# Kernel optimization log

Hardware: AMD Instinct MI355X
Metric: run time of the kernel (lower is better)

## Reference

```python
import jax, jax.numpy as jnp
import numpy as np

KH, KW, STRIDE, PAD, DIL = 3, 3, 1, 1, 1


def setup_inputs() -> dict:
    key = jax.random.key(0)
    ks = jax.random.split(key, 4)
    B, C, H, W, O = 4, 256, 64, 64, 256
    K = KH * KW
    x = jax.random.normal(ks[0], (B, C, H, W), jnp.float32)
    # offset/mask conv params (original inits to zero; use small random so offsets are non-trivial)
    w_om = jax.random.normal(ks[1], (3 * K, C, KH, KW), jnp.float32) * 0.01
    b_om = jnp.zeros((3 * K,), jnp.float32)
    # main weight: kaiming_uniform_(a=1) -> gain = sqrt(2/(1+1^2)) = 1, bound = sqrt(3)/sqrt(fan_in)
    fan_in = C * K
    bound = float(np.sqrt(3.0) / np.sqrt(fan_in))
    weight = jax.random.uniform(ks[2], (O, C, KH, KW), jnp.float32, -bound, bound)
    bias = jnp.zeros((O,), jnp.float32)
    return {"x": x, "w_om": w_om, "b_om": b_om, "weight": weight, "bias": bias}


def _deform_conv2d(x, offset, mask, weight, bias):
    # torchvision.ops.deform_conv2d semantics, deformable_groups=1, stride=1, pad=1, dil=1
    B, C, H, W = x.shape
    K = KH * KW
    # torchvision offset layout: per-tap interleaved (y, x) pairs along channel dim
    off_y = offset[:, 0::2]  # [B, K, H, W]
    off_x = offset[:, 1::2]  # [B, K, H, W]
    ky = (jnp.repeat(jnp.arange(KH), KW) * DIL).astype(x.dtype)  # [K]
    kx = (jnp.tile(jnp.arange(KW), KH) * DIL).astype(x.dtype)    # [K]
    base_y = (jnp.arange(H) * STRIDE - PAD).astype(x.dtype)
    base_x = (jnp.arange(W) * STRIDE - PAD).astype(x.dtype)
    py = base_y[None, None, :, None] + ky[None, :, None, None] + off_y  # [B,K,H,W]
    px = base_x[None, None, None, :] + kx[None, :, None, None] + off_x  # [B,K,H,W]
    y0 = jnp.floor(py)
    x0 = jnp.floor(px)
    ly = py - y0
    lx = px - x0
    y0i = y0.astype(jnp.int32)
    x0i = x0.astype(jnp.int32)
    x_flat = x.reshape(B, C, H * W)

    def gather(yy, xx):
        # zero-padded gather of one bilinear corner -> [B, C, K, H, W]
        valid = ((yy >= 0) & (yy < H) & (xx >= 0) & (xx < W)).astype(x.dtype)
        idx = (jnp.clip(yy, 0, H - 1) * W + jnp.clip(xx, 0, W - 1)).reshape(B, -1)
        g = jax.vmap(lambda xf, i: jnp.take(xf, i, axis=1))(x_flat, idx)
        return g.reshape(B, C, K, H, W) * valid.reshape(B, 1, K, H, W)

    w00 = ((1 - ly) * (1 - lx))[:, None]
    w01 = ((1 - ly) * lx)[:, None]
    w10 = (ly * (1 - lx))[:, None]
    w11 = (ly * lx)[:, None]
    val = (gather(y0i, x0i) * w00 + gather(y0i, x0i + 1) * w01
           + gather(y0i + 1, x0i) * w10 + gather(y0i + 1, x0i + 1) * w11)
    cols = val * mask[:, None]  # modulated columns [B,C,K,H,W]
    out = jnp.einsum('bckhw,ock->bohw', cols, weight.reshape(weight.shape[0], C, K))
    return out + bias[None, :, None, None]


def reference(x, w_om, b_om, weight, bias):
    om = jax.lax.conv_general_dilated(
        x, w_om, (STRIDE, STRIDE), ((PAD, PAD), (PAD, PAD)),
        rhs_dilation=(DIL, DIL), dimension_numbers=('NCHW', 'OIHW', 'NCHW'),
    ) + b_om[None, :, None, None]
    K = KH * KW
    o1, o2, m = om[:, :K], om[:, K:2 * K], om[:, 2 * K:]
    offset = jnp.concatenate([o1, o2], axis=1)  # [B, 2K, H, W]
    mask = jax.nn.sigmoid(m)                    # [B, K, H, W]
    return _deform_conv2d(x, offset, mask, weight, bias)
```

## Files before the change

kernel.cpp:

```cpp
#include <hip/hip_runtime.h>
#include <stdint.h>

#define B_ 4
#define C_ 256
#define H_ 64
#define W_ 64
#define O_ 256
#define K_ 9
#define CK 2304
#define HW 4096
#define NTOT 16384

typedef __bf16 bf16x8 __attribute__((ext_vector_type(8)));
typedef __bf16 bf16x4 __attribute__((ext_vector_type(4)));
typedef float f32x4 __attribute__((ext_vector_type(4)));
typedef float f32x2 __attribute__((ext_vector_type(2)));
typedef f32x2 __attribute__((aligned(4))) f32x2u;

__device__ __forceinline__ uint16_t f2bf(float f) {
  uint32_t u = __builtin_bit_cast(uint32_t, f);
  return (uint16_t)((u + 0x7FFFu + ((u >> 16) & 1u)) >> 16);
}

__device__ __forceinline__ uint32_t pk_bf16(float a, float b) {
  uint16_t lo = __builtin_bit_cast(uint16_t, (__bf16)a);
  uint16_t hi = __builtin_bit_cast(uint16_t, (__bf16)b);
  return (uint32_t)lo | ((uint32_t)hi << 16);
}

__global__ void kA_prep(const float* __restrict__ weight, const float* __restrict__ w_om,
                        const float* __restrict__ x, uint16_t* __restrict__ wb,
                        uint16_t* __restrict__ womb, uint16_t* __restrict__ xT) {
  int bx = blockIdx.x;
  int t = threadIdx.x;
  if (bx < 2304) {
    int idx = bx * 256 + t;
    int o = idx / CK;
    int rem = idx - o * CK;
    int k = rem >> 8, c = rem & 255;
    wb[idx] = f2bf(weight[(o * C_ + c) * K_ + k]);
  } else if (bx < 2592) {
    int idx = (bx - 2304) * 256 + t;
    int j = idx / CK;
    int ck = idx - j * CK;
    int k = ck >> 8, c = ck & 255;
    womb[idx] = (j < 27) ? f2bf(w_om[(j * 256 + c) * 9 + k]) : (uint16_t)0;
  } else {
    int bxl = bx - 2592;
    int ct = bxl & 3;
    int hwt = (bxl >> 2) & 63;
    int b = bxl >> 8;
    int l = t & 63;
    int cq = t >> 6;

    __shared__ __align__(16) uint16_t tile[64 * 72];

    const float* xb = x + ((b * 256 + ct * 64) * HW) + hwt * 64;
#pragma unroll
    for (int i = 0; i < 16; ++i) {
      int c = cq * 16 + i;
      tile[l * 72 + c] = f2bf(xb[c * HW + l]);
    }
    __syncthreads();

    int hw = t >> 2;
    int c8 = (t & 3) * 8;
    uint16_t* dst = xT + ((size_t)b << 20) + (size_t)(hwt * 64 + hw) * 256 + ct * 64;
    *(uint4*)&dst[c8] = *(const uint4*)&tile[hw * 72 + c8];
    *(uint4*)&dst[c8 + 32] = *(const uint4*)&tile[hw * 72 + c8 + 32];
  }
}

__device__ __forceinline__ void write_om(float v, int j, int n, const float* __restrict__ b_om,
                                         float* __restrict__ pypxmk) {
  if (j >= 27) return;
  float s = v + b_om[j];
  int b = n >> 12, hw = n & 4095;
  int h = hw >> 6, w = hw & 63;
  if (j < 18) {
    int k = j >> 1;
    int off = (b * 9 + k) * HW + hw;
    if ((j & 1) == 0)
      pypxmk[off] = (float)(h - 1 + k / 3) + s;
    else
      pypxmk[147456 + off] = (float)(w - 1 + k % 3) + s;
  } else {
    int k = j - 18;
    pypxmk[294912 + (b * 9 + k) * HW + hw] = 1.f / (1.f + __expf(-s));
  }
}

__global__ void k1_mfma(const uint16_t* __restrict__ womb, const uint16_t* __restrict__ xT,
                        const float* __restrict__ b_om, float* __restrict__ pypxmk) {
  int nt = blockIdx.x;
  int t = threadIdx.x;
  int lane = t & 63;
  int wid = t >> 6;
  int lr = lane & 15, q = lane >> 4;
  int n = nt * 64 + wid * 16 + lr;
  int b = n >> 12;
  int hw = n & 4095;
  int y = hw >> 6, xx = hw & 63;
  const uint16_t* xb = xT + ((size_t)b << 20);
  const uint16_t* zrow = womb + 31 * CK;

  f32x4 acc0 = {0.f, 0.f, 0.f, 0.f};
  f32x4 acc1 = {0.f, 0.f, 0.f, 0.f};

#pragma unroll
  for (int k = 0; k < 9; ++k) {
    int dy = k / 3, dx = k - dy * 3;
    int ny = y + dy - 1, nx = xx + dx - 1;
    bool valid = ((unsigned)ny < 64u) && ((unsigned)nx < 64u);
    int row = (min(max(ny, 0), 63) << 6) + min(max(nx, 0), 63);
    const uint16_t* bp = valid ? (xb + row * 256 + q * 8) : (zrow + q * 8);
    const uint16_t* ap = womb + lr * CK + k * 256 + q * 8;
#pragma unroll
    for (int kt = 0; kt < 8; ++kt) {
      int c0 = kt * 32;
      bf16x8 bF = *(const bf16x8*)&bp[c0];
      bf16x8 aF0 = *(const bf16x8*)&ap[c0];
      bf16x8 aF1 = *(const bf16x8*)&ap[16 * CK + c0];
      acc0 = __builtin_amdgcn_mfma_f32_16x16x32_bf16(aF0, bF, acc0, 0, 0, 0);
      acc1 = __builtin_amdgcn_mfma_f32_16x16x32_bf16(aF1, bF, acc1, 0, 0, 0);
    }
  }

#pragma unroll
  for (int r = 0; r < 4; ++r) {
    write_om(acc0[r], q * 4 + r, n, b_om, pypxmk);
    write_om(acc1[r], 16 + q * 4 + r, n, b_om, pypxmk);
  }
}


struct GatherState {
  float wa0[4], wb0[4], wa1[4], wb1[4];
  bf16x4 r00[4], r01[4], r10[4], r11[4];
};

__device__ __forceinline__ void gather_issue(GatherState& S, const uint16_t* __restrict__ xb,
                                             const float* __restrict__ pyA,
                                             const float* __restrict__ pxA,
                                             const float* __restrict__ mkA,
                                             int b, int kg, int n0, int rbase, int lane) {
#pragma unroll
  for (int j = 0; j < 4; ++j) {
    int nrow = rbase + j;
    int poff = (b * 9 + kg) * HW + ((n0 + nrow) & 4095);
    float py = pyA[poff];
    float px = pxA[poff];
    float mk = mkA[poff];
    float fy0 = floorf(py), fx0 = floorf(px);
    float ly = py - fy0, lx = px - fx0;
    int y0 = (int)fy0, x0 = (int)fx0;
    bool vy0 = ((unsigned)y0 < 64u), vy1 = ((unsigned)(y0 + 1) < 64u);
    bool vx0 = ((unsigned)x0 < 64u), vx1 = ((unsigned)(x0 + 1) < 64u);
    float w00 = (vy0 && vx0) ? (1.f - ly) * (1.f - lx) * mk : 0.f;
    float w01 = (vy0 && vx1) ? (1.f - ly) * lx * mk : 0.f;
    float w10 = (vy1 && vx0) ? ly * (1.f - lx) * mk : 0.f;
    float w11 = (vy1 && vx1) ? ly * lx * mk : 0.f;
    bool sel0 = (x0 >= 63);
    bool sel1 = (x0 >= 0);
    S.wa0[j] = (sel0 ? 0.f : w00) + (sel1 ? 0.f : w01);
    S.wb0[j] = (sel0 ? w00 : 0.f) + (sel1 ? w01 : 0.f);
    S.wa1[j] = (sel0 ? 0.f : w10) + (sel1 ? 0.f : w11);
    S.wb1[j] = (sel0 ? w10 : 0.f) + (sel1 ? w11 : 0.f);
    int bx0 = min(max(x0, 0), 62);
    int a0 = min(max(y0, 0), 63) * 64 + bx0;
    int a1 = min(max(y0 + 1, 0), 63) * 64 + bx0;
    S.r00[j] = *(const bf16x4*)&xb[a0 * 256 + lane * 4];
    S.r01[j] = *(const bf16x4*)&xb[a0 * 256 + 256 + lane * 4];
    S.r10[j] = *(const bf16x4*)&xb[a1 * 256 + lane * 4];
    S.r11[j] = *(const bf16x4*)&xb[a1 * 256 + 256 + lane * 4];
  }
}

__device__ __forceinline__ void gather_finish(const GatherState& S, uint16_t* bslab,
                                              int rbase, int lane) {
#pragma unroll
  for (int j = 0; j < 4; ++j) {
    int nrow = rbase + j;
    float v[4];
#pragma unroll
    for (int i = 0; i < 4; ++i)
      v[i] = S.wa0[j] * (float)S.r00[j][i] + S.wb0[j] * (float)S.r01[j][i] +
             S.wa1[j] * (float)S.r10[j][i] + S.wb1[j] * (float)S.r11[j][i];
    uint2 pk;
    pk.x = pk_bf16(v[0], v[1]);
    pk.y = pk_bf16(v[2], v[3]);
    int chunk = lane >> 1;
    int chs = (chunk & 24) | ((chunk & 7) ^ (nrow & 7));
    *(uint2*)&bslab[nrow * 256 + chs * 8 + (lane & 1) * 4] = pk;
  }
}

__device__ __forceinline__ void stageA(const uint16_t* __restrict__ wb, uint16_t* asbuf,
                                       int kbase, int t) {
#pragma unroll
  for (int i = 0; i < 4; ++i) {
    int rr = i * 64 + (t >> 3);
    const uint16_t* src = wb + rr * CK + kbase + (((t & 7) ^ (rr & 7)) << 3);
    __builtin_amdgcn_global_load_lds(
        (const __attribute__((address_space(1))) uint32_t*)src,
        (__attribute__((address_space(3))) uint32_t*)&asbuf[i * 4096 + t * 8], 16, 0, 0);
  }
}

__device__ __forceinline__ void mma_step(const uint16_t* AsP, const uint16_t* BsP,
                                         f32x4 acc[4][2], int wm, int wn, int lr, int q,
                                         int kt2) {
#pragma unroll
  for (int kc = 0; kc < 2; ++kc) {
    bf16x8 aF[4], bF[2];
#pragma unroll
    for (int i = 0; i < 4; ++i) {
      int row = wm * 64 + i * 16 + lr;
      aF[i] = *(const bf16x8*)&AsP[row * 64 + (((kc * 4 + q) ^ (row & 7)) << 3)];
    }
#pragma unroll
    for (int j = 0; j < 2; ++j) {
      int row = wn * 32 + j * 16 + lr;
      int kidx = kt2 * 8 + kc * 4 + q;
      int chs = (kidx & 24) | ((kidx & 7) ^ (row & 7));
      bF[j] = *(const bf16x8*)&BsP[row * 256 + chs * 8];
    }
#pragma unroll
    for (int i = 0; i < 4; ++i)
#pragma unroll
      for (int j = 0; j < 2; ++j)
        acc[i][j] = __builtin_amdgcn_mfma_f32_16x16x32_bf16(aF[i], bF[j], acc[i][j], 0, 0, 0);
  }
}

__global__ __launch_bounds__(512, 2) void k23_fused(const uint16_t* __restrict__ wb,
                                                    const uint16_t* __restrict__ xT,
                                                    const float* __restrict__ pypxmk,
                                                    const float* __restrict__ bias,
                                                    float* __restrict__ out) {
  __shared__ __align__(16) uint16_t As[2][16384];
  __shared__ __align__(16) uint16_t Bs[16384];

  int t = threadIdx.x;
  int lane = t & 63;
  int wid = __builtin_amdgcn_readfirstlane(t >> 6);
  int lr = lane & 15, q = lane >> 4;
  int wm = wid >> 1, wn = wid & 1;
  int bx = blockIdx.x;
  int swz = (bx & 7) * 32 + (bx >> 3);
  int n0 = swz * 64;
  int b = n0 >> 12;
  int hw0 = n0 & 4095;
  const uint16_t* xb = xT + ((size_t)b << 20);
  const float* pyA = pypxmk;
  const float* pxA = pypxmk + 147456;
  const float* mkA = pypxmk + 294912;

  f32x4 acc[4][2];
  const f32x4 zero = {0.f, 0.f, 0.f, 0.f};
#pragma unroll
  for (int i = 0; i < 4; ++i)
#pragma unroll
    for (int j = 0; j < 2; ++j) acc[i][j] = zero;

  GatherState S;
  int wrow = wid * 8;

  gather_issue(S, xb, pyA, pxA, mkA, b, 0, n0, wrow, lane);
  gather_finish(S, Bs, wrow, lane);
  gather_issue(S, xb, pyA, pxA, mkA, b, 0, n0, wrow + 4, lane);
  gather_finish(S, Bs, wrow + 4, lane);
  stageA(wb, As[0], 0, t);
  __syncthreads();

  for (int k = 0; k < 9; ++k) {
    for (int kt2 = 0; kt2 < 4; ++kt2) {
      if (!(k == 8 && kt2 == 3)) {
        int kb2 = (kt2 == 3) ? (k + 1) * 256 : k * 256 + (kt2 + 1) * 64;
        stageA(wb, As[(kt2 + 1) & 1], kb2, t);
      }
      mma_step(As[kt2 & 1], Bs, acc, wm, wn, lr, q, kt2);
      __syncthreads();
    }
    if (k < 8) {
      gather_issue(S, xb, pyA, pxA, mkA, b, k + 1, n0, wrow, lane);
      gather_finish(S, Bs, wrow, lane);
      gather_issue(S, xb, pyA, pxA, mkA, b, k + 1, n0, wrow + 4, lane);
      gather_finish(S, Bs, wrow + 4, lane);
      __syncthreads();
    }
  }

#pragma unroll
  for (int i = 0; i < 4; ++i) {
#pragma unroll
    for (int r = 0; r < 4; ++r) {
      int o = wm * 64 + i * 16 + q * 4 + r;
      float bv = bias[o];
      float* orow = out + (b * O_ + o) * HW + hw0;
#pragma unroll
      for (int j = 0; j < 2; ++j) orow[wn * 32 + j * 16 + lr] = acc[i][j][r] + bv;
    }
  }
}

__global__ void k0_wconv(const float* __restrict__ weight, uint16_t* __restrict__ wb) {
  int idx = blockIdx.x * 256 + threadIdx.x;
  if (idx >= O_ * CK) return;
  int o = idx / CK;
  int rem = idx - o * CK;
  int k = rem >> 8;
  int c = rem & 255;
  wb[idx] = f2bf(weight[(o * C_ + c) * K_ + k]);
}

__global__ void k1_offconv(const float* __restrict__ x, const float* __restrict__ w_om,
                           const float* __restrict__ b_om, float* __restrict__ pypxmk) {
  int bx = blockIdx.x;
  int jq = bx % 7;
  int h = (bx / 7) % H_;
  int b = bx / (7 * H_);
  int t = threadIdx.x;
  int w = t & 63;
  int cs = __builtin_amdgcn_readfirstlane(t >> 6);

  float acc[4] = {0.f, 0.f, 0.f, 0.f};
  const float* xb = x + (b * C_) * HW;

  for (int ci = 0; ci < 64; ++ci) {
    int c = cs * 64 + ci;
    const float* xr = xb + c * HW;
    float xv[3][3];
#pragma unroll
    for (int r = 0; r < 3; ++r) {
      int y = h - 1 + r;
      bool yv = ((unsigned)y < 64u);
#pragma unroll
      for (int dx = 0; dx < 3; ++dx) {
        int xx = w - 1 + dx;
        bool v = yv && ((unsigned)xx < 64u);
        xv[r][dx] = v ? xr[y * 64 + xx] : 0.f;
      }
    }
    const float* wp = w_om + ((jq * 4) * C_ + c) * 9;
#pragma unroll
    for (int jj = 0; jj < 4; ++jj) {
      int j = jq * 4 + jj;
      int jeff = (j < 27) ? jj : 0;
      const float* wj = wp + jeff * (C_ * 9);
      float a = 0.f;
#pragma unroll
      for (int r = 0; r < 3; ++r)
#pragma unroll
        for (int dx = 0; dx < 3; ++dx)
          a = fmaf(xv[r][dx], wj[r * 3 + dx], a);
      acc[jj] += a;
    }
  }

  __shared__ float red[4][4][64];
#pragma unroll
  for (int jj = 0; jj < 4; ++jj) red[cs][jj][w] = acc[jj];
  __syncthreads();

  int jj = t >> 6;
  int j = jq * 4 + jj;
  if (j < 27) {
    float s = red[0][jj][w] + red[1][jj][w] + red[2][jj][w] + red[3][jj][w] + b_om[j];
    float* pyA = pypxmk;
    float* pxA = pypxmk + 147456;
    float* mkA = pypxmk + 294912;
    if (j < 18) {
      int k = j >> 1;
      int off = (b * 9 + k) * HW + h * 64 + w;
      if ((j & 1) == 0)
        pyA[off] = (float)(h - 1 + k / 3) + s;
      else
        pxA[off] = (float)(w - 1 + k % 3) + s;
    } else {
      int k = j - 18;
      mkA[(b * 9 + k) * HW + h * 64 + w] = 1.f / (1.f + __expf(-s));
    }
  }
}

__global__ void k2_fb(const float* __restrict__ x, const float* __restrict__ pypxmk,
                      uint16_t* __restrict__ cols) {
  int bx = blockIdx.x;
  int cg = bx & 15;
  int h = (bx >> 4) & 63;
  int b = bx >> 10;
  int t = threadIdx.x;
  int w = t & 63;
  int g = t >> 6;

  const float* pyA = pypxmk;
  const float* pxA = pypxmk + 147456;
  const float* mkA = pypxmk + 294912;

  __shared__ uint16_t tile[64 * 146];
  const float* xb = x + b * C_ * HW;
  int cbase = cg * 16 + g * 4;

#pragma unroll
  for (int k = 0; k < 9; ++k) {
    int poff = (b * 9 + k) * HW + h * 64 + w;
    float py = pyA[poff];
    float px = pxA[poff];
    float mk = mkA[poff];
    float fy0 = floorf(py), fx0 = floorf(px);
    float ly = py - fy0, lx = px - fx0;
    int y0 = (int)fy0, x0 = (int)fx0;
    bool vy0 = ((unsigned)y0 < 64u), vy1 = ((unsigned)(y0 + 1) < 64u);
    bool vx0 = ((unsigned)x0 < 64u), vx1 = ((unsigned)(x0 + 1) < 64u);
    float w00 = (vy0 && vx0) ? (1.f - ly) * (1.f - lx) * mk : 0.f;
    float w01 = (vy0 && vx1) ? (1.f - ly) * lx * mk : 0.f;
    float w10 = (vy1 && vx0) ? ly * (1.f - lx) * mk : 0.f;
    float w11 = (vy1 && vx1) ? ly * lx * mk : 0.f;
    bool sel0 = (x0 >= 63);
    bool sel1 = (x0 >= 0);
    float wa0 = (sel0 ? 0.f : w00) + (sel1 ? 0.f : w01);
    float wb0 = (sel0 ? w00 : 0.f) + (sel1 ? w01 : 0.f);
    float wa1 = (sel0 ? 0.f : w10) + (sel1 ? 0.f : w11);
    float wb1 = (sel0 ? w10 : 0.f) + (sel1 ? w11 : 0.f);
    int bx0 = min(max(x0, 0), 62);
    int a0 = min(max(y0, 0), 63) * 64 + bx0;
    int a1 = min(max(y0 + 1, 0), 63) * 64 + bx0;

#pragma unroll
    for (int cp = 0; cp < 2; ++cp) {
      const float* xcA = xb + (cbase + cp * 2) * HW;
      const float* xcB = xcA + HW;
      f32x2 A0 = *(const f32x2u*)&xcA[a0];
      f32x2 A1 = *(const f32x2u*)&xcA[a1];
      f32x2 B0 = *(const f32x2u*)&xcB[a0];
      f32x2 B1 = *(const f32x2u*)&xcB[a1];
      float rA = wa0 * A0.x + wb0 * A0.y + wa1 * A1.x + wb1 * A1.y;
      float rB = wa0 * B0.x + wb0 * B0.y + wa1 * B1.x + wb1 * B1.y;
      *(uint32_t*)&tile[w * 146 + k * 16 + g * 4 + cp * 2] = pk_bf16(rA, rB);
    }
  }
  __syncthreads();

#pragma unroll
  for (int it = 0; it < 18; ++it) {
    int u = t + it * 256;
    int wu = u / 72;
    int rem = u - wu * 72;
    int k = rem >> 3;
    int cd = rem & 7;
    uint32_t val = *(const uint32_t*)&tile[wu * 146 + rem * 2];
    int n = b * HW + h * 64 + wu;
    int dst = n * CK + k * 256 + cg * 16 + cd * 2;
    *(uint32_t*)&cols[dst] = val;
  }
}

__global__ void k3_flex(const uint16_t* __restrict__ wb, const uint16_t* __restrict__ cols,
                        const float* __restrict__ bias, float* __restrict__ out) {
  int bx = blockIdx.x;
  int mt = bx & 1;
  int nt = bx >> 1;
  int o0 = mt * 128;
  int n0 = nt * 128;
  int t = threadIdx.x;
  int lane = t & 63;
  int wid = t >> 6;
  int wm = wid >> 1, wn = wid & 1;
  int lr = lane & 15, q = lane >> 4;

  __shared__ __align__(16) uint16_t As[128 * 32];
  __shared__ __align__(16) uint16_t Bs[128 * 32];

  f32x4 acc[4][4];
  const f32x4 zero = {0.f, 0.f, 0.f, 0.f};
#pragma unroll
  for (int i = 0; i < 4; ++i)
#pragma unroll
    for (int j = 0; j < 4; ++j) acc[i][j] = zero;

  int r0 = t >> 2;
  int koff = (t & 3) * 8;
  const uint16_t* gA = wb + (o0 + r0) * CK + koff;
  const uint16_t* gB = cols + (n0 + r0) * CK + koff;

  for (int kt = 0; kt < 72; ++kt) {
    int k0 = kt * 32;
    __builtin_amdgcn_global_load_lds(
        (const __attribute__((address_space(1))) uint32_t*)(gA + k0),
        (__attribute__((address_space(3))) uint32_t*)&As[t * 8], 16, 0, 0);
    __builtin_amdgcn_global_load_lds(
        (const __attribute__((address_space(1))) uint32_t*)(gA + 64 * CK + k0),
        (__attribute__((address_space(3))) uint32_t*)&As[2048 + t * 8], 16, 0, 0);
    __builtin_amdgcn_global_load_lds(
        (const __attribute__((address_space(1))) uint32_t*)(gB + k0),
        (__attribute__((address_space(3))) uint32_t*)&Bs[t * 8], 16, 0, 0);
    __builtin_amdgcn_global_load_lds(
        (const __attribute__((address_space(1))) uint32_t*)(gB + 64 * CK + k0),
        (__attribute__((address_space(3))) uint32_t*)&Bs[2048 + t * 8], 16, 0, 0);
    __syncthreads();

    bf16x8 aF[4], bF[4];
#pragma unroll
    for (int i = 0; i < 4; ++i)
      aF[i] = *(const bf16x8*)&As[(wm * 64 + i * 16 + lr) * 32 + q * 8];
#pragma unroll
    for (int j = 0; j < 4; ++j)
      bF[j] = *(const bf16x8*)&Bs[(wn * 64 + j * 16 + lr) * 32 + q * 8];
#pragma unroll
    for (int i = 0; i < 4; ++i)
#pragma unroll
      for (int j = 0; j < 4; ++j)
        acc[i][j] = __builtin_amdgcn_mfma_f32_16x16x32_bf16(aF[i], bF[j], acc[i][j], 0, 0, 0);
    __syncthreads();
  }

  int bb = n0 >> 12;
  int hw0 = n0 & 4095;
#pragma unroll
  for (int i = 0; i < 4; ++i) {
#pragma unroll
    for (int r = 0; r < 4; ++r) {
      int o = o0 + wm * 64 + i * 16 + q * 4 + r;
      float bv = bias[o];
      float* orow = out + (bb * O_ + o) * HW + hw0;
#pragma unroll
      for (int j = 0; j < 4; ++j) orow[wn * 64 + j * 16 + lr] = acc[i][j][r] + bv;
    }
  }
}

extern "C" void kernel_launch(void* const* d_in, const int* in_sizes, int n_in,
                              void* d_out, int out_size, void* d_ws, size_t ws_size,
                              hipStream_t stream) {
  const float* x = (const float*)d_in[0];
  const float* w_om = (const float*)d_in[1];
  const float* b_om = (const float*)d_in[2];
  const float* weight = (const float*)d_in[3];
  const float* bias = (const float*)d_in[4];
  float* out = (float*)d_out;

  char* ws = (char*)d_ws;
  uint16_t* wb = (uint16_t*)ws;
  uint16_t* womb = (uint16_t*)(ws + 1179648);
  uint16_t* xT = (uint16_t*)(ws + 1327104);
  float* pypxmk = (float*)(ws + 9715712);

  if (ws_size >= 11485184ull) {
    hipLaunchKernelGGL(kA_prep, dim3(3616), dim3(256), 0, stream, weight, w_om, x, wb, womb, xT);
    hipLaunchKernelGGL(k1_mfma, dim3(256), dim3(256), 0, stream, womb, xT, b_om, pypxmk);
    hipLaunchKernelGGL(k23_fused, dim3(256), dim3(512), 0, stream, wb, xT, pypxmk, bias, out);
  } else {
    float* pypx_fb = (float*)(ws + 1179648);
    uint16_t* colsf = (uint16_t*)(ws + 2949120);
    hipLaunchKernelGGL(k0_wconv, dim3(2304), dim3(256), 0, stream, weight, wb);
    hipLaunchKernelGGL(k1_offconv, dim3(4 * 64 * 7), dim3(256), 0, stream, x, w_om, b_om, pypx_fb);
    hipLaunchKernelGGL(k2_fb, dim3(4 * 64 * 16), dim3(256), 0, stream, x, pypx_fb, colsf);
    hipLaunchKernelGGL(k3_flex, dim3(256), dim3(256), 0, stream, wb, colsf, bias, out);
  }
}
```

Before: 168.9 us.

## Fuse offset/mask conv into deformable GEMM kernel and compact weight prep

The offset/mask convolution moves out of its own kernel and into the start of the fused gather+GEMM kernel. Each block computes the offsets for its 64 output positions with MFMA, splitting the 9 taps across two wave halves and reducing them through shared memory. The results stay in LDS instead of going through a global pypxmk buffer, which removes one launch and a global round trip. The weight conversion in the prep kernel is also restructured so each thread converts 9 taps per channel, cutting the grid size. The cost is some offset-conv work at the head of each block, which adds latency before the gather pipeline can start.

```diff
diff --git a/kernel.cpp b/kernel.cpp
--- a/kernel.cpp
+++ b/kernel.cpp
@@ -33,20 +33,22 @@
                         uint16_t* __restrict__ womb, uint16_t* __restrict__ xT) {
   int bx = blockIdx.x;
   int t = threadIdx.x;
-  if (bx < 2304) {
-    int idx = bx * 256 + t;
-    int o = idx / CK;
-    int rem = idx - o * CK;
-    int k = rem >> 8, c = rem & 255;
-    wb[idx] = f2bf(weight[(o * C_ + c) * K_ + k]);
-  } else if (bx < 2592) {
-    int idx = (bx - 2304) * 256 + t;
-    int j = idx / CK;
-    int ck = idx - j * CK;
-    int k = ck >> 8, c = ck & 255;
-    womb[idx] = (j < 27) ? f2bf(w_om[(j * 256 + c) * 9 + k]) : (uint16_t)0;
+  if (bx < 256) {
+    int o = bx, c = t;
+    const float* wp = weight + (o * 256 + c) * 9;
+#pragma unroll
+    for (int k = 0; k < 9; ++k) wb[o * CK + k * 256 + c] = f2bf(wp[k]);
+  } else if (bx < 283) {
+    int j = bx - 256, c = t;
+    const float* wp = w_om + (j * 256 + c) * 9;
+#pragma unroll
+    for (int k = 0; k < 9; ++k) womb[j * CK + k * 256 + c] = f2bf(wp[k]);
+  } else if (bx < 288) {
+    int j = 27 + (bx - 283), c = t;
+#pragma unroll
+    for (int k = 0; k < 9; ++k) womb[j * CK + k * 256 + c] = 0;
   } else {
-    int bxl = bx - 2592;
+    int bxl = bx - 288;
     int ct = bxl & 3;
     int hwt = (bxl >> 2) & 63;
     int b = bxl >> 8;
@@ -71,68 +73,6 @@
   }
 }
 
-__device__ __forceinline__ void write_om(float v, int j, int n, const float* __restrict__ b_om,
-                                         float* __restrict__ pypxmk) {
-  if (j >= 27) return;
-  float s = v + b_om[j];
-  int b = n >> 12, hw = n & 4095;
-  int h = hw >> 6, w = hw & 63;
-  if (j < 18) {
-    int k = j >> 1;
-    int off = (b * 9 + k) * HW + hw;
-    if ((j & 1) == 0)
-      pypxmk[off] = (float)(h - 1 + k / 3) + s;
-    else
-      pypxmk[147456 + off] = (float)(w - 1 + k % 3) + s;
-  } else {
-    int k = j - 18;
-    pypxmk[294912 + (b * 9 + k) * HW + hw] = 1.f / (1.f + __expf(-s));
-  }
-}
-
-__global__ void k1_mfma(const uint16_t* __restrict__ womb, const uint16_t* __restrict__ xT,
-                        const float* __restrict__ b_om, float* __restrict__ pypxmk) {
-  int nt = blockIdx.x;
-  int t = threadIdx.x;
-  int lane = t & 63;
-  int wid = t >> 6;
-  int lr = lane & 15, q = lane >> 4;
-  int n = nt * 64 + wid * 16 + lr;
-  int b = n >> 12;
-  int hw = n & 4095;
-  int y = hw >> 6, xx = hw & 63;
-  const uint16_t* xb = xT + ((size_t)b << 20);
-  const uint16_t* zrow = womb + 31 * CK;
-
-  f32x4 acc0 = {0.f, 0.f, 0.f, 0.f};
-  f32x4 acc1 = {0.f, 0.f, 0.f, 0.f};
-
-#pragma unroll
-  for (int k = 0; k < 9; ++k) {
-    int dy = k / 3, dx = k - dy * 3;
-    int ny = y + dy - 1, nx = xx + dx - 1;
-    bool valid = ((unsigned)ny < 64u) && ((unsigned)nx < 64u);
-    int row = (min(max(ny, 0), 63) << 6) + min(max(nx, 0), 63);
-    const uint16_t* bp = valid ? (xb + row * 256 + q * 8) : (zrow + q * 8);
-    const uint16_t* ap = womb + lr * CK + k * 256 + q * 8;
-#pragma unroll
-    for (int kt = 0; kt < 8; ++kt) {
-      int c0 = kt * 32;
-      bf16x8 bF = *(const bf16x8*)&bp[c0];
-      bf16x8 aF0 = *(const bf16x8*)&ap[c0];
-      bf16x8 aF1 = *(const bf16x8*)&ap[16 * CK + c0];
-      acc0 = __builtin_amdgcn_mfma_f32_16x16x32_bf16(aF0, bF, acc0, 0, 0, 0);
-      acc1 = __builtin_amdgcn_mfma_f32_16x16x32_bf16(aF1, bF, acc1, 0, 0, 0);
-    }
-  }
-
-#pragma unroll
-  for (int r = 0; r < 4; ++r) {
-    write_om(acc0[r], q * 4 + r, n, b_om, pypxmk);
-    write_om(acc1[r], 16 + q * 4 + r, n, b_om, pypxmk);
-  }
-}
-
 
 struct GatherState {
   float wa0[4], wb0[4], wa1[4], wb1[4];
@@ -140,17 +80,14 @@
 };
 
 __device__ __forceinline__ void gather_issue(GatherState& S, const uint16_t* __restrict__ xb,
-                                             const float* __restrict__ pyA,
-                                             const float* __restrict__ pxA,
-                                             const float* __restrict__ mkA,
-                                             int b, int kg, int n0, int rbase, int lane) {
+                                             const float* pypx_l,
+                                             int kg, int rbase, int lane) {
 #pragma unroll
   for (int j = 0; j < 4; ++j) {
     int nrow = rbase + j;
-    int poff = (b * 9 + kg) * HW + ((n0 + nrow) & 4095);
-    float py = pyA[poff];
-    float px = pxA[poff];
-    float mk = mkA[poff];
+    float py = pypx_l[(0 * 9 + kg) * 64 + nrow];
+    float px = pypx_l[(1 * 9 + kg) * 64 + nrow];
+    float mk = pypx_l[(2 * 9 + kg) * 64 + nrow];
     float fy0 = floorf(py), fx0 = floorf(px);
     float ly = py - fy0, lx = px - fx0;
     int y0 = (int)fy0, x0 = (int)fx0;
@@ -233,28 +170,90 @@
   }
 }
 
-__global__ __launch_bounds__(512, 2) void k23_fused(const uint16_t* __restrict__ wb,
-                                                    const uint16_t* __restrict__ xT,
-                                                    const float* __restrict__ pypxmk,
-                                                    const float* __restrict__ bias,
-                                                    float* __restrict__ out) {
+__global__ __launch_bounds__(512, 2) void k123(const uint16_t* __restrict__ wb,
+                                               const uint16_t* __restrict__ womb,
+                                               const uint16_t* __restrict__ xT,
+                                               const float* __restrict__ b_om,
+                                               const float* __restrict__ bias,
+                                               float* __restrict__ out) {
   __shared__ __align__(16) uint16_t As[2][16384];
   __shared__ __align__(16) uint16_t Bs[16384];
+  __shared__ float pypx_l[3 * 9 * 64];
 
   int t = threadIdx.x;
   int lane = t & 63;
   int wid = __builtin_amdgcn_readfirstlane(t >> 6);
   int lr = lane & 15, q = lane >> 4;
-  int wm = wid >> 1, wn = wid & 1;
   int bx = blockIdx.x;
   int swz = (bx & 7) * 32 + (bx >> 3);
   int n0 = swz * 64;
   int b = n0 >> 12;
   int hw0 = n0 & 4095;
   const uint16_t* xb = xT + ((size_t)b << 20);
-  const float* pyA = pypxmk;
-  const float* pxA = pypxmk + 147456;
-  const float* mkA = pypxmk + 294912;
+
+  {
+    int ns4 = wid & 3;
+    int kh2 = wid >> 2;
+    int hw = (n0 + ns4 * 16 + lr) & 4095;
+    int y = hw >> 6, xx = hw & 63;
+    const uint16_t* zrow = womb + 31 * CK;
+
+    f32x4 acc0 = {0.f, 0.f, 0.f, 0.f};
+    f32x4 acc1 = {0.f, 0.f, 0.f, 0.f};
+
+    int ks = kh2 ? 4 : 0;
+    int ke = kh2 ? 9 : 4;
+    for (int k = ks; k < ke; ++k) {
+      int dy = k / 3, dx = k - dy * 3;
+      int ny = y + dy - 1, nx = xx + dx - 1;
+      bool valid = ((unsigned)ny < 64u) && ((unsigned)nx < 64u);
+      int row = (min(max(ny, 0), 63) << 6) + min(max(nx, 0), 63);
+      const uint16_t* bp = valid ? (xb + row * 256 + q * 8) : (zrow + q * 8);
+      const uint16_t* ap = womb + lr * CK + k * 256 + q * 8;
+#pragma unroll
+      for (int kt = 0; kt < 8; ++kt) {
+        int c0 = kt * 32;
+        bf16x8 bF = *(const bf16x8*)&bp[c0];
+        bf16x8 aF0 = *(const bf16x8*)&ap[c0];
+        bf16x8 aF1 = *(const bf16x8*)&ap[16 * CK + c0];
+        acc0 = __builtin_amdgcn_mfma_f32_16x16x32_bf16(aF0, bF, acc0, 0, 0, 0);
+        acc1 = __builtin_amdgcn_mfma_f32_16x16x32_bf16(aF1, bF, acc1, 0, 0, 0);
+      }
+    }
+
+    float* red = (float*)As;
+    int base = ((kh2 * 4 + ns4) * 64 + lane) * 8;
+#pragma unroll
+    for (int r = 0; r < 4; ++r) {
+      red[base + r] = acc0[r];
+      red[base + 4 + r] = acc1[r];
+    }
+    __syncthreads();
+
+    if (kh2 == 0) {
+      int b0 = (ns4 * 64 + lane) * 8;
+      int b1 = ((4 + ns4) * 64 + lane) * 8;
+      int nn = ns4 * 16 + lr;
+#pragma unroll
+      for (int i = 0; i < 8; ++i) {
+        float s = red[b0 + i] + red[b1 + i];
+        int j = (i < 4) ? (q * 4 + i) : (16 + q * 4 + (i - 4));
+        if (j < 27) {
+          float v = s + b_om[j];
+          if (j < 18) {
+            int k = j >> 1;
+            if ((j & 1) == 0)
+              pypx_l[(0 * 9 + k) * 64 + nn] = (float)(y - 1 + k / 3) + v;
+            else
+              pypx_l[(1 * 9 + k) * 64 + nn] = (float)(xx - 1 + k % 3) + v;
+          } else {
+            pypx_l[(2 * 9 + (j - 18)) * 64 + nn] = 1.f / (1.f + __expf(-v));
+          }
+        }
+      }
+    }
+    __syncthreads();
+  }
 
   f32x4 acc[4][2];
   const f32x4 zero = {0.f, 0.f, 0.f, 0.f};
@@ -263,12 +262,13 @@
 #pragma unroll
     for (int j = 0; j < 2; ++j) acc[i][j] = zero;
 
+  int wm = wid >> 1, wn = wid & 1;
   GatherState S;
   int wrow = wid * 8;
 
-  gather_issue(S, xb, pyA, pxA, mkA, b, 0, n0, wrow, lane);
+  gather_issue(S, xb, pypx_l, 0, wrow, lane);
   gather_finish(S, Bs, wrow, lane);
-  gather_issue(S, xb, pyA, pxA, mkA, b, 0, n0, wrow + 4, lane);
+  gather_issue(S, xb, pypx_l, 0, wrow + 4, lane);
   gather_finish(S, Bs, wrow + 4, lane);
   stageA(wb, As[0], 0, t);
   __syncthreads();
@@ -283,9 +283,9 @@
       __syncthreads();
     }
     if (k < 8) {
-      gather_issue(S, xb, pyA, pxA, mkA, b, k + 1, n0, wrow, lane);
+      gather_issue(S, xb, pypx_l, k + 1, wrow, lane);
       gather_finish(S, Bs, wrow, lane);
-      gather_issue(S, xb, pyA, pxA, mkA, b, k + 1, n0, wrow + 4, lane);
+      gather_issue(S, xb, pypx_l, k + 1, wrow + 4, lane);
       gather_finish(S, Bs, wrow + 4, lane);
       __syncthreads();
     }
@@ -387,7 +387,7 @@
 __global__ void k2_fb(const float* __restrict__ x, const float* __restrict__ pypxmk,
                       uint16_t* __restrict__ cols) {
   int bx = blockIdx.x;
-  int cg = bx & 15;
+  int cg2 = bx & 15;
   int h = (bx >> 4) & 63;
   int b = bx >> 10;
   int t = threadIdx.x;
@@ -400,7 +400,7 @@
 
   __shared__ uint16_t tile[64 * 146];
   const float* xb = x + b * C_ * HW;
-  int cbase = cg * 16 + g * 4;
+  int cbase = cg2 * 16 + g * 4;
 
 #pragma unroll
   for (int k = 0; k < 9; ++k) {
@@ -451,7 +451,7 @@
     int cd = rem & 7;
     uint32_t val = *(const uint32_t*)&tile[wu * 146 + rem * 2];
     int n = b * HW + h * 64 + wu;
-    int dst = n * CK + k * 256 + cg * 16 + cd * 2;
+    int dst = n * CK + k * 256 + cg2 * 16 + cd * 2;
     *(uint32_t*)&cols[dst] = val;
   }
 }
@@ -544,12 +544,10 @@
   uint16_t* wb = (uint16_t*)ws;
   uint16_t* womb = (uint16_t*)(ws + 1179648);
   uint16_t* xT = (uint16_t*)(ws + 1327104);
-  float* pypxmk = (float*)(ws + 9715712);
 
   if (ws_size >= 11485184ull) {
-    hipLaunchKernelGGL(kA_prep, dim3(3616), dim3(256), 0, stream, weight, w_om, x, wb, womb, xT);
-    hipLaunchKernelGGL(k1_mfma, dim3(256), dim3(256), 0, stream, womb, xT, b_om, pypxmk);
-    hipLaunchKernelGGL(k23_fused, dim3(256), dim3(512), 0, stream, wb, xT, pypxmk, bias, out);
+    hipLaunchKernelGGL(kA_prep, dim3(1312), dim3(256), 0, stream, weight, w_om, x, wb, womb, xT);
+    hipLaunchKernelGGL(k123, dim3(256), dim3(512), 0, stream, wb, womb, xT, b_om, bias, out);
   } else {
     float* pypx_fb = (float*)(ws + 1179648);
     uint16_t* colsf = (uint16_t*)(ws + 2949120);
```

New measurement: 158.7 us. 6.1% less time.
